# Kernel tuning notes

Hardware: AMD Instinct MI355X
Metric: run time of the kernel (lower is better)

The kernel has to match this reference:

```python
import jax, jax.numpy as jnp
import numpy as np

TS = 6      # texture cube size (hard-coded in module)
S = 256     # image size (NMR default / ref image size)
DIST = 2.732


def _look_at(verts, eye):
    # NMR look_at: camera at eye, looking at origin, up=(0,1,0)
    eye = jnp.asarray(eye, verts.dtype)
    z = -eye / jnp.linalg.norm(eye)
    up = jnp.array([0.0, 1.0, 0.0], verts.dtype)
    x = jnp.cross(up, z)
    x = x / jnp.linalg.norm(x)
    y = jnp.cross(z, x)
    R = jnp.stack([x, y, z])          # rows = camera axes
    return (verts - eye) @ R.T


def _render(verts, faces, tex_flat, eye):
    # verts [V,3], faces [F,3] int, tex_flat [F*TS^3, 3] (tanh already applied)
    v = _look_at(verts, eye)
    fv = v[faces]                      # [F,3,3]
    p0, p1, p2 = fv[:, 0], fv[:, 1], fv[:, 2]
    ps = (2.0 * jnp.arange(S, dtype=verts.dtype) + 1.0 - S) / S
    PX = jnp.broadcast_to(ps[None, :], (S, S)).reshape(-1)      # x right
    PY = jnp.broadcast_to(-ps[:, None], (S, S)).reshape(-1)     # y up (row 0 = top)

    def edge(a, b):
        # signed edge function, [F,HW]
        return ((PX[None, :] - a[:, 0:1]) * (b[:, 1:2] - a[:, 1:2])
                - (PY[None, :] - a[:, 1:2]) * (b[:, 0:1] - a[:, 0:1]))

    e0 = edge(p1, p2)
    e1 = edge(p2, p0)
    e2 = edge(p0, p1)
    # per-face signed area (double area) [F,1]
    area = ((p1[:, 0] - p0[:, 0]) * (p2[:, 1] - p0[:, 1])
            - (p1[:, 1] - p0[:, 1]) * (p2[:, 0] - p0[:, 0]))[:, None]
    ok = jnp.abs(area) > 1e-8
    inv = jnp.where(ok, 1.0 / jnp.where(ok, area, 1.0), 0.0)
    w0, w1, w2 = e0 * inv, e1 * inv, e2 * inv            # barycentric weights
    inside = (w0 >= 0) & (w1 >= 0) & (w2 >= 0) & ok       # both windings (fill_back)
    z = w0 * p0[:, 2:3] + w1 * p1[:, 2:3] + w2 * p2[:, 2:3]
    depth = jnp.where(inside & (z > 0), z, jnp.inf)       # z-buffer candidates
    best = jnp.argmin(depth, axis=0)                      # [HW] winning face
    hit = jnp.take_along_axis(depth, best[None, :], axis=0)[0] < jnp.inf
    wb = jnp.stack([jnp.take_along_axis(w, best[None, :], axis=0)[0]
                    for w in (w0, w1, w2)], axis=-1)       # [HW,3]
    ti = jnp.clip(jnp.round(wb * (TS - 1)), 0, TS - 1).astype(jnp.int32)
    flat = ((best * TS + ti[:, 0]) * TS + ti[:, 1]) * TS + ti[:, 2]
    colors = tex_flat[flat]                                # [HW,3] gather
    img = jnp.where(hit[:, None], colors, 0.0)
    return img.reshape(S, S, 3).transpose(2, 0, 1)[None]   # [1,3,S,S]


def setup_inputs() -> dict:
    key = jax.random.key(0)
    k1, k2, k3, k4, k5 = jax.random.split(key, 5)
    V, F = 252, 500
    return {
        "vertices": jax.random.normal(k1, (1, V, 3), jnp.float32),
        "faces": jax.random.randint(k2, (1, F, 3), 0, V, jnp.int64),
        "textures": jax.random.normal(k3, (1, F, TS, TS, TS, 3), jnp.float32),
        "image_ref": jax.random.uniform(k4, (1, 3, S, S), jnp.float32),
        "image_ref_2": jax.random.uniform(k5, (1, 3, S, S), jnp.float32),
    }


def reference(vertices, faces, textures, image_ref, image_ref_2):
    tex_flat = jnp.tanh(textures[0]).reshape(-1, 3)
    v, f = vertices[0], faces[0]
    # eye = get_points_from_angles(2.732, 180, 0) -> (0, 0, +d)
    img1 = _render(v, f, tex_flat, jnp.array([0.0, 0.0, DIST], jnp.float32))
    loss_one_side = jnp.sum((img1 - image_ref) ** 2)
    # eye = get_points_from_angles(2.732, 0, 0) -> (0, 0, -d)
    img2 = _render(v, f, tex_flat, jnp.array([0.0, 0.0, -DIST], jnp.float32))
    loss_symmetric = jnp.sum((img2 - image_ref_2) ** 2)
    return (loss_one_side + loss_symmetric) / 2
```

## Files before the change

kernel.cpp:

```cpp
#include <hip/hip_runtime.h>
#include <math.h>

#define IMG_S 256
#define NFACE 500
#define TSZ 6
#define DIST 2.732f


__device__ __forceinline__ void edge_coef(float ax, float ay, float bx, float by,
                                          float inv, float& A, float& B, float& C) {
    float dy = by - ay;
    float dx = bx - ax;
    A = dy * inv;
    B = -dx * inv;
    C = (ay * dx - ax * dy) * inv;
}

__global__ __launch_bounds__(256) void render_loss_kernel(
    const float* __restrict__ verts,
    const int*   __restrict__ faces,
    const float* __restrict__ tex,
    const float* __restrict__ ref0,
    const float* __restrict__ ref1,
    float*       __restrict__ partials)
{
    __shared__ float4 fc[NFACE][3];
    __shared__ float red[4];

    const int view = blockIdx.y;

    for (int f = threadIdx.x; f < NFACE; f += blockDim.x) {
        int i0 = faces[f * 3 + 0];
        int i1 = faces[f * 3 + 1];
        int i2 = faces[f * 3 + 2];

        float v0x = verts[i0 * 3 + 0], v0y = verts[i0 * 3 + 1], v0z = verts[i0 * 3 + 2];
        float v1x = verts[i1 * 3 + 0], v1y = verts[i1 * 3 + 1], v1z = verts[i1 * 3 + 2];
        float v2x = verts[i2 * 3 + 0], v2y = verts[i2 * 3 + 1], v2z = verts[i2 * 3 + 2];

        float p0x, p0y, p0z, p1x, p1y, p1z, p2x, p2y, p2z;
        if (view == 0) {
            p0x = -v0x; p0y = v0y; p0z = DIST - v0z;
            p1x = -v1x; p1y = v1y; p1z = DIST - v1z;
            p2x = -v2x; p2y = v2y; p2z = DIST - v2z;
        } else {
            p0x = v0x; p0y = v0y; p0z = v0z + DIST;
            p1x = v1x; p1y = v1y; p1z = v1z + DIST;
            p2x = v2x; p2y = v2y; p2z = v2z + DIST;
        }

        float area = (p1x - p0x) * (p2y - p0y) - (p1y - p0y) * (p2x - p0x);
        bool ok = fabsf(area) > 1e-8f;

        float A0, B0, C0, A1, B1, C1, A2, B2, C2, Az, Bz, Cz;
        if (ok) {
            float inv = 1.0f / area;
            edge_coef(p1x, p1y, p2x, p2y, inv, A0, B0, C0);
            edge_coef(p2x, p2y, p0x, p0y, inv, A1, B1, C1);
            edge_coef(p0x, p0y, p1x, p1y, inv, A2, B2, C2);
            Az = A0 * p0z + A1 * p1z + A2 * p2z;
            Bz = B0 * p0z + B1 * p1z + B2 * p2z;
            Cz = C0 * p0z + C1 * p1z + C2 * p2z;
        } else {
            A0 = B0 = A1 = B1 = A2 = B2 = 0.0f;
            C0 = C1 = C2 = -1.0f;
            Az = Bz = 0.0f; Cz = 0.0f;
        }
        fc[f][0] = make_float4(A0, B0, C0, A1);
        fc[f][1] = make_float4(B1, C1, A2, B2);
        fc[f][2] = make_float4(C2, Az, Bz, Cz);
    }
    __syncthreads();

    const int pix = blockIdx.x * blockDim.x + threadIdx.x;
    const int ix = pix & (IMG_S - 1);
    const int iy = pix >> 8;
    const float px = (2.0f * (float)ix + 1.0f - (float)IMG_S) * (1.0f / (float)IMG_S);
    const float py = -((2.0f * (float)iy + 1.0f - (float)IMG_S) * (1.0f / (float)IMG_S));

    float bestz = INFINITY;
    int besti = -1;

    for (int f = 0; f < NFACE; ++f) {
        float4 q0 = fc[f][0];
        float4 q1 = fc[f][1];
        float4 q2 = fc[f][2];
        float w0 = fmaf(px, q0.x, fmaf(py, q0.y, q0.z));
        float w1 = fmaf(px, q0.w, fmaf(py, q1.x, q1.y));
        float w2 = fmaf(px, q1.z, fmaf(py, q1.w, q2.x));
        float z  = fmaf(px, q2.y, fmaf(py, q2.z, q2.w));
        float wmin = fminf(w0, fminf(w1, w2));
        bool c = (wmin >= 0.0f) && (z > 0.0f) && (z < bestz);
        bestz = c ? z : bestz;
        besti = c ? f : besti;
    }

    float c0 = 0.0f, c1 = 0.0f, c2 = 0.0f;
    if (besti >= 0) {
        float4 q0 = fc[besti][0];
        float4 q1 = fc[besti][1];
        float4 q2 = fc[besti][2];
        float w0 = fmaf(px, q0.x, fmaf(py, q0.y, q0.z));
        float w1 = fmaf(px, q0.w, fmaf(py, q1.x, q1.y));
        float w2 = fmaf(px, q1.z, fmaf(py, q1.w, q2.x));
        int t0 = (int)fminf(fmaxf(rintf(w0 * (float)(TSZ - 1)), 0.0f), (float)(TSZ - 1));
        int t1 = (int)fminf(fmaxf(rintf(w1 * (float)(TSZ - 1)), 0.0f), (float)(TSZ - 1));
        int t2 = (int)fminf(fmaxf(rintf(w2 * (float)(TSZ - 1)), 0.0f), (float)(TSZ - 1));
        int flat = ((besti * TSZ + t0) * TSZ + t1) * TSZ + t2;
        const float* t = tex + (long)flat * 3;
        c0 = tanhf(t[0]);
        c1 = tanhf(t[1]);
        c2 = tanhf(t[2]);
    }

    const float* __restrict__ ref = (view == 0) ? ref0 : ref1;
    float d0 = c0 - ref[0 * IMG_S * IMG_S + pix];
    float d1 = c1 - ref[1 * IMG_S * IMG_S + pix];
    float d2 = c2 - ref[2 * IMG_S * IMG_S + pix];
    float acc = fmaf(d0, d0, fmaf(d1, d1, d2 * d2));

    for (int off = 32; off > 0; off >>= 1)
        acc += __shfl_down(acc, off, 64);
    int lane = threadIdx.x & 63;
    int wid = threadIdx.x >> 6;
    if (lane == 0) red[wid] = acc;
    __syncthreads();
    if (threadIdx.x == 0) {
        partials[blockIdx.y * gridDim.x + blockIdx.x] = red[0] + red[1] + red[2] + red[3];
    }
}

__global__ __launch_bounds__(256) void reduce_kernel(const float* __restrict__ partials,
                                                     int n, float* __restrict__ out) {
    __shared__ float red[4];
    float v = 0.0f;
    for (int i = threadIdx.x; i < n; i += 256) v += partials[i];
    for (int off = 32; off > 0; off >>= 1)
        v += __shfl_down(v, off, 64);
    int lane = threadIdx.x & 63;
    int wid = threadIdx.x >> 6;
    if (lane == 0) red[wid] = v;
    __syncthreads();
    if (threadIdx.x == 0) {
        out[0] = 0.5f * (red[0] + red[1] + red[2] + red[3]);
    }
}

extern "C" void kernel_launch(void* const* d_in, const int* in_sizes, int n_in,
                              void* d_out, int out_size, void* d_ws, size_t ws_size,
                              hipStream_t stream) {
    const float* verts = (const float*)d_in[0];
    const int*   faces = (const int*)d_in[1];
    const float* tex   = (const float*)d_in[2];
    const float* ref0  = (const float*)d_in[3];
    const float* ref1  = (const float*)d_in[4];
    float* out = (float*)d_out;
    float* partials = (float*)d_ws;

    const int blocks_per_view = (IMG_S * IMG_S) / 256;
    dim3 grid(blocks_per_view, 2);
    render_loss_kernel<<<grid, 256, 0, stream>>>(verts, faces, tex, ref0, ref1, partials);
    reduce_kernel<<<1, 256, 0, stream>>>(partials, blocks_per_view * 2, out);
}
```

Baseline: 97.52 us.

## Split face loop into chunks across blocks with packed depth-index min merge

Rasterization is split across four face chunks in separate blocks, each writing a packed (depth bits, face index) 64-bit word per pixel. A second kernel takes the minimum over the chunks, recomputes the winning face's coefficients, shades and computes the loss. This gives four times more blocks and a shorter serial loop per thread, and shrinks shared-memory setup per block. In exchange it adds global traffic for the packed buffer and an extra kernel launch. The depth test is also rewritten as a single min-based comparison.

Result: faster. 93.78 us (-3.8%).

```diff
diff --git a/kernel.cpp b/kernel.cpp
--- a/kernel.cpp
+++ b/kernel.cpp
@@ -2,10 +2,16 @@
 #include <math.h>
 
 #define IMG_S 256
+#define NPIX (IMG_S * IMG_S)
 #define NFACE 500
+#define NCHUNK 4
+#define FPC (NFACE / NCHUNK)
 #define TSZ 6
 #define DIST 2.732f
 
+struct FaceCoef {
+    float A0, B0, C0, A1, B1, C1, A2, B2, C2, Az, Bz, Cz;
+};
 
 __device__ __forceinline__ void edge_coef(float ax, float ay, float bx, float by,
                                           float inv, float& A, float& B, float& C) {
@@ -16,72 +22,81 @@
     C = (ay * dx - ax * dy) * inv;
 }
 
-__global__ __launch_bounds__(256) void render_loss_kernel(
+__device__ __forceinline__ FaceCoef compute_face(const float* __restrict__ verts,
+                                                 const int* __restrict__ faces,
+                                                 int f, int view) {
+    int i0 = faces[f * 3 + 0];
+    int i1 = faces[f * 3 + 1];
+    int i2 = faces[f * 3 + 2];
+
+    float v0x = verts[i0 * 3 + 0], v0y = verts[i0 * 3 + 1], v0z = verts[i0 * 3 + 2];
+    float v1x = verts[i1 * 3 + 0], v1y = verts[i1 * 3 + 1], v1z = verts[i1 * 3 + 2];
+    float v2x = verts[i2 * 3 + 0], v2y = verts[i2 * 3 + 1], v2z = verts[i2 * 3 + 2];
+
+    float p0x, p0y, p0z, p1x, p1y, p1z, p2x, p2y, p2z;
+    if (view == 0) {
+        p0x = -v0x; p0y = v0y; p0z = DIST - v0z;
+        p1x = -v1x; p1y = v1y; p1z = DIST - v1z;
+        p2x = -v2x; p2y = v2y; p2z = DIST - v2z;
+    } else {
+        p0x = v0x; p0y = v0y; p0z = v0z + DIST;
+        p1x = v1x; p1y = v1y; p1z = v1z + DIST;
+        p2x = v2x; p2y = v2y; p2z = v2z + DIST;
+    }
+
+    float area = (p1x - p0x) * (p2y - p0y) - (p1y - p0y) * (p2x - p0x);
+    bool ok = fabsf(area) > 1e-8f;
+
+    FaceCoef fc;
+    if (ok) {
+        float inv = 1.0f / area;
+        edge_coef(p1x, p1y, p2x, p2y, inv, fc.A0, fc.B0, fc.C0);
+        edge_coef(p2x, p2y, p0x, p0y, inv, fc.A1, fc.B1, fc.C1);
+        edge_coef(p0x, p0y, p1x, p1y, inv, fc.A2, fc.B2, fc.C2);
+        fc.Az = fc.A0 * p0z + fc.A1 * p1z + fc.A2 * p2z;
+        fc.Bz = fc.B0 * p0z + fc.B1 * p1z + fc.B2 * p2z;
+        fc.Cz = fc.C0 * p0z + fc.C1 * p1z + fc.C2 * p2z;
+    } else {
+        fc.A0 = fc.B0 = fc.A1 = fc.B1 = fc.A2 = fc.B2 = 0.0f;
+        fc.C0 = fc.C1 = fc.C2 = -1.0f;
+        fc.Az = fc.Bz = fc.Cz = 0.0f;
+    }
+    return fc;
+}
+
+__device__ __forceinline__ float pix_x(int ix) {
+    return (2.0f * (float)ix + 1.0f - (float)IMG_S) * (1.0f / (float)IMG_S);
+}
+__device__ __forceinline__ float pix_y(int iy) {
+    return -((2.0f * (float)iy + 1.0f - (float)IMG_S) * (1.0f / (float)IMG_S));
+}
+
+__global__ __launch_bounds__(256) void raster_chunk_kernel(
     const float* __restrict__ verts,
     const int*   __restrict__ faces,
-    const float* __restrict__ tex,
-    const float* __restrict__ ref0,
-    const float* __restrict__ ref1,
-    float*       __restrict__ partials)
+    unsigned long long* __restrict__ packed_out)
 {
-    __shared__ float4 fc[NFACE][3];
-    __shared__ float red[4];
-
-    const int view = blockIdx.y;
-
-    for (int f = threadIdx.x; f < NFACE; f += blockDim.x) {
-        int i0 = faces[f * 3 + 0];
-        int i1 = faces[f * 3 + 1];
-        int i2 = faces[f * 3 + 2];
-
-        float v0x = verts[i0 * 3 + 0], v0y = verts[i0 * 3 + 1], v0z = verts[i0 * 3 + 2];
-        float v1x = verts[i1 * 3 + 0], v1y = verts[i1 * 3 + 1], v1z = verts[i1 * 3 + 2];
-        float v2x = verts[i2 * 3 + 0], v2y = verts[i2 * 3 + 1], v2z = verts[i2 * 3 + 2];
-
-        float p0x, p0y, p0z, p1x, p1y, p1z, p2x, p2y, p2z;
-        if (view == 0) {
-            p0x = -v0x; p0y = v0y; p0z = DIST - v0z;
-            p1x = -v1x; p1y = v1y; p1z = DIST - v1z;
-            p2x = -v2x; p2y = v2y; p2z = DIST - v2z;
-        } else {
-            p0x = v0x; p0y = v0y; p0z = v0z + DIST;
-            p1x = v1x; p1y = v1y; p1z = v1z + DIST;
-            p2x = v2x; p2y = v2y; p2z = v2z + DIST;
-        }
-
-        float area = (p1x - p0x) * (p2y - p0y) - (p1y - p0y) * (p2x - p0x);
-        bool ok = fabsf(area) > 1e-8f;
-
-        float A0, B0, C0, A1, B1, C1, A2, B2, C2, Az, Bz, Cz;
-        if (ok) {
-            float inv = 1.0f / area;
-            edge_coef(p1x, p1y, p2x, p2y, inv, A0, B0, C0);
-            edge_coef(p2x, p2y, p0x, p0y, inv, A1, B1, C1);
-            edge_coef(p0x, p0y, p1x, p1y, inv, A2, B2, C2);
-            Az = A0 * p0z + A1 * p1z + A2 * p2z;
-            Bz = B0 * p0z + B1 * p1z + B2 * p2z;
-            Cz = C0 * p0z + C1 * p1z + C2 * p2z;
-        } else {
-            A0 = B0 = A1 = B1 = A2 = B2 = 0.0f;
-            C0 = C1 = C2 = -1.0f;
-            Az = Bz = 0.0f; Cz = 0.0f;
-        }
-        fc[f][0] = make_float4(A0, B0, C0, A1);
-        fc[f][1] = make_float4(B1, C1, A2, B2);
-        fc[f][2] = make_float4(C2, Az, Bz, Cz);
+    __shared__ float4 fc[FPC][3];
+    const int chunk = blockIdx.y;
+    const int view  = blockIdx.z;
+    const int fbase = chunk * FPC;
+
+    if (threadIdx.x < FPC) {
+        FaceCoef c = compute_face(verts, faces, fbase + (int)threadIdx.x, view);
+        fc[threadIdx.x][0] = make_float4(c.A0, c.B0, c.C0, c.A1);
+        fc[threadIdx.x][1] = make_float4(c.B1, c.C1, c.A2, c.B2);
+        fc[threadIdx.x][2] = make_float4(c.C2, c.Az, c.Bz, c.Cz);
     }
     __syncthreads();
 
     const int pix = blockIdx.x * blockDim.x + threadIdx.x;
-    const int ix = pix & (IMG_S - 1);
-    const int iy = pix >> 8;
-    const float px = (2.0f * (float)ix + 1.0f - (float)IMG_S) * (1.0f / (float)IMG_S);
-    const float py = -((2.0f * (float)iy + 1.0f - (float)IMG_S) * (1.0f / (float)IMG_S));
+    const float px = pix_x(pix & (IMG_S - 1));
+    const float py = pix_y(pix >> 8);
 
     float bestz = INFINITY;
     int besti = -1;
 
-    for (int f = 0; f < NFACE; ++f) {
+    for (int f = 0; f < FPC; ++f) {
         float4 q0 = fc[f][0];
         float4 q1 = fc[f][1];
         float4 q2 = fc[f][2];
@@ -90,23 +105,56 @@
         float w2 = fmaf(px, q1.z, fmaf(py, q1.w, q2.x));
         float z  = fmaf(px, q2.y, fmaf(py, q2.z, q2.w));
         float wmin = fminf(w0, fminf(w1, w2));
-        bool c = (wmin >= 0.0f) && (z > 0.0f) && (z < bestz);
+        float s = fminf(z, bestz - z);
+        bool c = (wmin >= 0.0f) && (s > 0.0f);
         bestz = c ? z : bestz;
         besti = c ? f : besti;
     }
 
+    unsigned long long packed;
+    if (besti >= 0)
+        packed = ((unsigned long long)__float_as_uint(bestz) << 32) |
+                 (unsigned int)(fbase + besti);
+    else
+        packed = ~0ull;
+    packed_out[(size_t)(view * NCHUNK + chunk) * NPIX + pix] = packed;
+}
+
+__global__ __launch_bounds__(256) void shade_loss_kernel(
+    const float* __restrict__ verts,
+    const int*   __restrict__ faces,
+    const float* __restrict__ tex,
+    const float* __restrict__ ref0,
+    const float* __restrict__ ref1,
+    const unsigned long long* __restrict__ packed_in,
+    float* __restrict__ partials)
+{
+    __shared__ float red[4];
+    const int gid  = blockIdx.x * blockDim.x + threadIdx.x;
+    const int view = gid >> 16;
+    const int pix  = gid & (NPIX - 1);
+
+    const unsigned long long* p = packed_in + (size_t)view * NCHUNK * NPIX + pix;
+    unsigned long long best = p[0];
+    #pragma unroll
+    for (int c = 1; c < NCHUNK; ++c) {
+        unsigned long long v = p[(size_t)c * NPIX];
+        best = (v < best) ? v : best;
+    }
+
     float c0 = 0.0f, c1 = 0.0f, c2 = 0.0f;
-    if (besti >= 0) {
-        float4 q0 = fc[besti][0];
-        float4 q1 = fc[besti][1];
-        float4 q2 = fc[besti][2];
-        float w0 = fmaf(px, q0.x, fmaf(py, q0.y, q0.z));
-        float w1 = fmaf(px, q0.w, fmaf(py, q1.x, q1.y));
-        float w2 = fmaf(px, q1.z, fmaf(py, q1.w, q2.x));
+    if (best != ~0ull) {
+        int fidx = (int)(best & 0xFFFFFFFFu);
+        FaceCoef fcw = compute_face(verts, faces, fidx, view);
+        const float px = pix_x(pix & (IMG_S - 1));
+        const float py = pix_y(pix >> 8);
+        float w0 = fmaf(px, fcw.A0, fmaf(py, fcw.B0, fcw.C0));
+        float w1 = fmaf(px, fcw.A1, fmaf(py, fcw.B1, fcw.C1));
+        float w2 = fmaf(px, fcw.A2, fmaf(py, fcw.B2, fcw.C2));
         int t0 = (int)fminf(fmaxf(rintf(w0 * (float)(TSZ - 1)), 0.0f), (float)(TSZ - 1));
         int t1 = (int)fminf(fmaxf(rintf(w1 * (float)(TSZ - 1)), 0.0f), (float)(TSZ - 1));
         int t2 = (int)fminf(fmaxf(rintf(w2 * (float)(TSZ - 1)), 0.0f), (float)(TSZ - 1));
-        int flat = ((besti * TSZ + t0) * TSZ + t1) * TSZ + t2;
+        int flat = ((fidx * TSZ + t0) * TSZ + t1) * TSZ + t2;
         const float* t = tex + (long)flat * 3;
         c0 = tanhf(t[0]);
         c1 = tanhf(t[1]);
@@ -114,9 +162,9 @@
     }
 
     const float* __restrict__ ref = (view == 0) ? ref0 : ref1;
-    float d0 = c0 - ref[0 * IMG_S * IMG_S + pix];
-    float d1 = c1 - ref[1 * IMG_S * IMG_S + pix];
-    float d2 = c2 - ref[2 * IMG_S * IMG_S + pix];
+    float d0 = c0 - ref[0 * NPIX + pix];
+    float d1 = c1 - ref[1 * NPIX + pix];
+    float d2 = c2 - ref[2 * NPIX + pix];
     float acc = fmaf(d0, d0, fmaf(d1, d1, d2 * d2));
 
     for (int off = 32; off > 0; off >>= 1)
@@ -125,9 +173,8 @@
     int wid = threadIdx.x >> 6;
     if (lane == 0) red[wid] = acc;
     __syncthreads();
-    if (threadIdx.x == 0) {
-        partials[blockIdx.y * gridDim.x + blockIdx.x] = red[0] + red[1] + red[2] + red[3];
-    }
+    if (threadIdx.x == 0)
+        partials[blockIdx.x] = red[0] + red[1] + red[2] + red[3];
 }
 
 __global__ __launch_bounds__(256) void reduce_kernel(const float* __restrict__ partials,
@@ -141,9 +188,8 @@
     int wid = threadIdx.x >> 6;
     if (lane == 0) red[wid] = v;
     __syncthreads();
-    if (threadIdx.x == 0) {
+    if (threadIdx.x == 0)
         out[0] = 0.5f * (red[0] + red[1] + red[2] + red[3]);
-    }
 }
 
 extern "C" void kernel_launch(void* const* d_in, const int* in_sizes, int n_in,
@@ -155,10 +201,15 @@
     const float* ref0  = (const float*)d_in[3];
     const float* ref1  = (const float*)d_in[4];
     float* out = (float*)d_out;
-    float* partials = (float*)d_ws;
-
-    const int blocks_per_view = (IMG_S * IMG_S) / 256;
-    dim3 grid(blocks_per_view, 2);
-    render_loss_kernel<<<grid, 256, 0, stream>>>(verts, faces, tex, ref0, ref1, partials);
-    reduce_kernel<<<1, 256, 0, stream>>>(partials, blocks_per_view * 2, out);
-}
+
+    unsigned long long* packed = (unsigned long long*)d_ws;
+    float* partials = (float*)((char*)d_ws + (size_t)2 * NCHUNK * NPIX * 8);
+
+    dim3 grid1(NPIX / 256, NCHUNK, 2);
+    raster_chunk_kernel<<<grid1, 256, 0, stream>>>(verts, faces, packed);
+
+    const int shade_blocks = (2 * NPIX) / 256;
+    shade_loss_kernel<<<shade_blocks, 256, 0, stream>>>(verts, faces, tex, ref0, ref1,
+                                                        packed, partials);
+    reduce_kernel<<<1, 256, 0, stream>>>(partials, shade_blocks, out);
+}
```
